# Kernel tuning notes

Hardware: AMD Instinct MI355X
Metric: run time of the kernel (lower is better)

The kernel has to match this reference:

```python
import jax, jax.numpy as jnp
import numpy as np

N_ENTITIES = 300000
N_ITEMS = 150000
N_USERS = 150000
N_EDGES = 2000000
N_INTER = 2000000
N_REL = 32
D = 64


def _scatter_mean(src, index, dim_size):
    # torch_scatter.scatter_mean: sum per segment divided by count; empty segments -> 0
    sums = jax.ops.segment_sum(src, index, num_segments=dim_size)
    cnt = jax.ops.segment_sum(jnp.ones((src.shape[0],), src.dtype), index, num_segments=dim_size)
    return sums / jnp.maximum(cnt, 1.0)[:, None]


def setup_inputs() -> dict:
    key = jax.random.key(0)
    ks = jax.random.split(key, 9)
    return {
        "entity_emb": jax.random.normal(ks[0], (N_ENTITIES, D), dtype=jnp.float32),
        "user_emb": jax.random.normal(ks[1], (N_USERS, D), dtype=jnp.float32),
        "edge_index": jax.random.randint(ks[2], (2, N_EDGES), 0, N_ENTITIES),
        "edge_type": jax.random.randint(ks[3], (N_EDGES,), 0, N_REL),
        "mat_row": jax.random.randint(ks[4], (N_INTER,), 0, N_USERS),
        "mat_col": jax.random.randint(ks[5], (N_INTER,), 0, N_ITEMS),
        "weight": jax.random.normal(ks[6], (N_REL, D), dtype=jnp.float32),
        "gate1_w": jax.random.normal(ks[7], (D, D), dtype=jnp.float32) * 0.1,
        "gate2_w": jax.random.normal(ks[8], (D, D), dtype=jnp.float32) * 0.1,
    }


def reference(entity_emb, user_emb, edge_index, edge_type, mat_row, mat_col, weight, gate1_w, gate2_w):
    head, tail = edge_index[0], edge_index[1]
    # KG aggregation: gather tail embeddings, modulate by relation emb, scatter-mean to head
    neigh_relation_emb = entity_emb[tail] * weight[edge_type]          # [E, D]
    entity_kg_agg = _scatter_mean(neigh_relation_emb, head, N_ENTITIES)
    item_kg_agg = entity_kg_agg[:N_ITEMS]                              # [I, D]
    att_kg_agg = entity_kg_agg[N_ITEMS:]                               # [Ent-I, D]
    # interaction aggregation: gather user emb by row, scatter-mean to item (col)
    item_int_agg = _scatter_mean(user_emb[mat_row], mat_col, N_ITEMS)  # [I, D]
    # gated fusion (F.linear: x @ W.T)
    gi = jax.nn.sigmoid(item_kg_agg @ gate1_w.T + item_int_agg @ gate2_w.T)
    item_emb_fusion = gi * item_kg_agg + (1.0 - gi) * item_int_agg
    # sparse mm with all-ones values == segment sum of fused item embs over users
    user_agg = jax.ops.segment_sum(item_emb_fusion[mat_col], mat_row, num_segments=N_USERS)
    final_entity_agg = jnp.concatenate([item_emb_fusion, att_kg_agg], axis=0)
    return (final_entity_agg, user_agg, item_kg_agg, item_int_agg)
```

## Files before the change

kernel.cpp:

```cpp
#include <hip/hip_runtime.h>

#define N_ENTITIES 300000
#define N_ITEMS    150000
#define N_USERS    150000
#define N_EDGES    2000000
#define N_INTER    2000000
#define D          64
#define N_TOT      (N_ENTITIES + N_ITEMS + N_USERS)

__global__ void hist_ent_kernel(const int* __restrict__ head,
                                int* __restrict__ cnt,
                                int* __restrict__ r_ent) {
    int e = blockIdx.x * 256 + threadIdx.x;
    if (e >= N_EDGES) return;
    r_ent[e] = atomicAdd(&cnt[head[e]], 1);
}

__global__ void hist_item_kernel(const int* __restrict__ mat_col,
                                 int* __restrict__ cnt,
                                 int* __restrict__ r_item) {
    int e = blockIdx.x * 256 + threadIdx.x;
    if (e >= N_INTER) return;
    r_item[e] = atomicAdd(&cnt[N_ENTITIES + mat_col[e]], 1);
}

__global__ void hist_user_kernel(const int* __restrict__ mat_row,
                                 int* __restrict__ cnt,
                                 int* __restrict__ r_user) {
    int e = blockIdx.x * 256 + threadIdx.x;
    if (e >= N_INTER) return;
    r_user[e] = atomicAdd(&cnt[N_ENTITIES + N_ITEMS + mat_row[e]], 1);
}

__global__ void transpose_gates_kernel(const float* __restrict__ g1,
                                       const float* __restrict__ g2,
                                       float* __restrict__ g1t,
                                       float* __restrict__ g2t) {
    int i = blockIdx.x * 256 + threadIdx.x;
    if (i >= 64 * 64) return;
    int o = i >> 6, k = i & 63;
    g1t[k * 64 + o] = g1[i];
    g2t[k * 64 + o] = g2[i];
}

__global__ __launch_bounds__(256) void scan_partial(const int* __restrict__ in,
                                                    int* __restrict__ incl,
                                                    int* __restrict__ bsums,
                                                    int n) {
    __shared__ int lds[256];
    int t = threadIdx.x;
    int base = blockIdx.x * 1024 + t * 4;
    int v0 = (base + 0 < n) ? in[base + 0] : 0;
    int v1 = (base + 1 < n) ? in[base + 1] : 0;
    int v2 = (base + 2 < n) ? in[base + 2] : 0;
    int v3 = (base + 3 < n) ? in[base + 3] : 0;
    int s = v0 + v1 + v2 + v3;
    lds[t] = s;
    __syncthreads();
    for (int off = 1; off < 256; off <<= 1) {
        int x = (t >= off) ? lds[t - off] : 0;
        __syncthreads();
        lds[t] += x;
        __syncthreads();
    }
    int excl = lds[t] - s;
    if (base + 0 < n) incl[base + 0] = excl + v0;
    if (base + 1 < n) incl[base + 1] = excl + v0 + v1;
    if (base + 2 < n) incl[base + 2] = excl + v0 + v1 + v2;
    if (base + 3 < n) incl[base + 3] = excl + s;
    if (t == 255) bsums[blockIdx.x] = lds[255];
}

__global__ __launch_bounds__(1024) void scan_bsums(int* __restrict__ bsums, int nb) {
    __shared__ int lds[1024];
    int t = threadIdx.x;
    lds[t] = (t < nb) ? bsums[t] : 0;
    __syncthreads();
    for (int off = 1; off < 1024; off <<= 1) {
        int x = (t >= off) ? lds[t - off] : 0;
        __syncthreads();
        lds[t] += x;
        __syncthreads();
    }
    if (t < nb) bsums[t] = lds[t];
}

__global__ void scan_finalize(const int* __restrict__ incl,
                              const int* __restrict__ bsums,
                              int* __restrict__ off_ent,
                              int* __restrict__ off_item,
                              int* __restrict__ off_user) {
    int i = blockIdx.x * 256 + threadIdx.x;
    if (i >= N_TOT) return;
    int b = i >> 10;
    int g = incl[i] + ((b > 0) ? bsums[b - 1] : 0);
    if (i < N_ENTITIES) {
        off_ent[i + 1] = g;
        if (i == 0) { off_ent[0] = 0; }
    } else if (i < N_ENTITIES + N_ITEMS) {
        off_item[i - N_ENTITIES + 1] = g - N_EDGES;
        if (i == N_ENTITIES) { off_item[0] = 0; }
    } else {
        off_user[i - N_ENTITIES - N_ITEMS + 1] = g - 2 * N_EDGES;
        if (i == N_ENTITIES + N_ITEMS) { off_user[0] = 0; }
    }
}

__global__ void scatter_ent_kernel(const int* __restrict__ head,
                                   const int* __restrict__ tail,
                                   const int* __restrict__ type,
                                   const int* __restrict__ r_ent,
                                   const int* __restrict__ off_ent,
                                   int* __restrict__ tt_sorted) {
    int e = blockIdx.x * 256 + threadIdx.x;
    if (e >= N_EDGES) return;
    int pos = off_ent[head[e]] + r_ent[e];
    __builtin_nontemporal_store(tail[e] | (type[e] << 19), &tt_sorted[pos]);
}

__global__ void scatter_item_kernel(const int* __restrict__ mat_col,
                                    const int* __restrict__ mat_row,
                                    const int* __restrict__ r_item,
                                    const int* __restrict__ off_item,
                                    int* __restrict__ row_sorted) {
    int e = blockIdx.x * 256 + threadIdx.x;
    if (e >= N_INTER) return;
    int pos = off_item[mat_col[e]] + r_item[e];
    __builtin_nontemporal_store(mat_row[e], &row_sorted[pos]);
}

__global__ void scatter_user_kernel(const int* __restrict__ mat_row,
                                    const int* __restrict__ mat_col,
                                    const int* __restrict__ r_user,
                                    const int* __restrict__ off_user,
                                    int* __restrict__ col_sorted) {
    int e = blockIdx.x * 256 + threadIdx.x;
    if (e >= N_INTER) return;
    int pos = off_user[mat_row[e]] + r_user[e];
    __builtin_nontemporal_store(mat_col[e], &col_sorted[pos]);
}

__global__ __launch_bounds__(256, 8) void agg_ent_kernel(
        const float* __restrict__ entity_emb, const float* __restrict__ weight,
        const int* __restrict__ off, const int* __restrict__ tt_sorted,
        float* __restrict__ out_item_kg, float* __restrict__ out_final) {
    int wave = threadIdx.x >> 6, lane = threadIdx.x & 63;
    int g = lane >> 4, q = lane & 15;
    int ent = blockIdx.x * 4 + wave;
    if (ent >= N_ENTITIES) return;
    int s = off[ent], e = off[ent + 1];
    int cnt = e - s;
    const float4* __restrict__ emb4 = (const float4*)entity_emb;
    const float4* __restrict__ wt4  = (const float4*)weight;
    float ax = 0.f, ay = 0.f, az = 0.f, aw = 0.f;
    for (int idx = s + g; idx < e; idx += 8) {
        int v0 = tt_sorted[idx];
        int i2 = idx + 4;
        bool p2 = (i2 < e);
        int v1 = p2 ? tt_sorted[i2] : 0;
        {
            int t = v0 & 0x7FFFF, w = v0 >> 19;
            float4 a = emb4[t * 16 + q];
            float4 b = wt4[w * 16 + q];
            ax += a.x * b.x; ay += a.y * b.y; az += a.z * b.z; aw += a.w * b.w;
        }
        if (p2) {
            int t = v1 & 0x7FFFF, w = v1 >> 19;
            float4 a = emb4[t * 16 + q];
            float4 b = wt4[w * 16 + q];
            ax += a.x * b.x; ay += a.y * b.y; az += a.z * b.z; aw += a.w * b.w;
        }
    }
    ax += __shfl_xor(ax, 16); ax += __shfl_xor(ax, 32);
    ay += __shfl_xor(ay, 16); ay += __shfl_xor(ay, 32);
    az += __shfl_xor(az, 16); az += __shfl_xor(az, 32);
    aw += __shfl_xor(aw, 16); aw += __shfl_xor(aw, 32);
    if (g == 0) {
        float inv = 1.0f / (float)(cnt > 1 ? cnt : 1);
        float4 r; r.x = ax * inv; r.y = ay * inv; r.z = az * inv; r.w = aw * inv;
        if (ent < N_ITEMS) ((float4*)out_item_kg)[ent * 16 + q] = r;
        else               ((float4*)out_final)[ent * 16 + q]   = r;
    }
}

__global__ __launch_bounds__(512, 6) void agg_item_fuse_kernel(
        const float* __restrict__ user_emb,
        const int* __restrict__ off, const int* __restrict__ row_sorted,
        const float* __restrict__ item_kg,
        const float* __restrict__ g1t, const float* __restrict__ g2t,
        float* __restrict__ out_item_int, float* __restrict__ out_final) {
    __shared__ float s_g1t[4096];
    __shared__ float s_g2t[4096];
    __shared__ float s_ii[8 * 64];

    {
        const float4* a = (const float4*)g1t;
        const float4* b = (const float4*)g2t;
        float4* sa = (float4*)s_g1t;
        float4* sb = (float4*)s_g2t;
        #pragma unroll
        for (int i = threadIdx.x; i < 1024; i += 512) { sa[i] = a[i]; sb[i] = b[i]; }
    }

    int wave = threadIdx.x >> 6, lane = threadIdx.x & 63;
    int g = lane >> 4, q = lane & 15;
    int item = blockIdx.x * 8 + wave;
    int s = off[item], e = off[item + 1];
    int cnt = e - s;
    const float4* __restrict__ ue4 = (const float4*)user_emb;
    float ax = 0.f, ay = 0.f, az = 0.f, aw = 0.f;
    for (int idx = s + g; idx < e; idx += 8) {
        int r0 = row_sorted[idx];
        int i2 = idx + 4;
        bool p2 = (i2 < e);
        int r1 = p2 ? row_sorted[i2] : 0;
        {
            float4 v = ue4[r0 * 16 + q];
            ax += v.x; ay += v.y; az += v.z; aw += v.w;
        }
        if (p2) {
            float4 v = ue4[r1 * 16 + q];
            ax += v.x; ay += v.y; az += v.z; aw += v.w;
        }
    }
    ax += __shfl_xor(ax, 16); ax += __shfl_xor(ax, 32);
    ay += __shfl_xor(ay, 16); ay += __shfl_xor(ay, 32);
    az += __shfl_xor(az, 16); az += __shfl_xor(az, 32);
    aw += __shfl_xor(aw, 16); aw += __shfl_xor(aw, 32);
    float inv = 1.0f / (float)(cnt > 1 ? cnt : 1);
    ax *= inv; ay *= inv; az *= inv; aw *= inv;
    if (g == 0) {
        float4 t; t.x = ax; t.y = ay; t.z = az; t.w = aw;
        *(float4*)&s_ii[wave * 64 + 4 * q] = t;
    }
    __syncthreads();

    const float* __restrict__ kgrow = item_kg + (long long)item * 64;
    float gx = 0.f, gy = 0.f, gz = 0.f, gw = 0.f;
    #pragma unroll 4
    for (int i = 0; i < 16; ++i) {
        int k = 16 * g + i;
        float kk = kgrow[k];
        float ik = s_ii[wave * 64 + k];
        float4 w1 = *(const float4*)&s_g1t[k * 64 + 4 * q];
        float4 w2 = *(const float4*)&s_g2t[k * 64 + 4 * q];
        gx += kk * w1.x + ik * w2.x;
        gy += kk * w1.y + ik * w2.y;
        gz += kk * w1.z + ik * w2.z;
        gw += kk * w1.w + ik * w2.w;
    }
    gx += __shfl_xor(gx, 16); gx += __shfl_xor(gx, 32);
    gy += __shfl_xor(gy, 16); gy += __shfl_xor(gy, 32);
    gz += __shfl_xor(gz, 16); gz += __shfl_xor(gz, 32);
    gw += __shfl_xor(gw, 16); gw += __shfl_xor(gw, 32);

    if (g == 0) {
        float4 kg4 = *(const float4*)&kgrow[4 * q];
        float4 ii4; ii4.x = ax; ii4.y = ay; ii4.z = az; ii4.w = aw;
        float4 o;
        float s0 = 1.0f / (1.0f + __expf(-gx)); o.x = s0 * kg4.x + (1.0f - s0) * ii4.x;
        float s1 = 1.0f / (1.0f + __expf(-gy)); o.y = s1 * kg4.y + (1.0f - s1) * ii4.y;
        float s2 = 1.0f / (1.0f + __expf(-gz)); o.z = s2 * kg4.z + (1.0f - s2) * ii4.z;
        float s3 = 1.0f / (1.0f + __expf(-gw)); o.w = s3 * kg4.w + (1.0f - s3) * ii4.w;
        ((float4*)out_item_int)[item * 16 + q] = ii4;
        ((float4*)out_final)[item * 16 + q]    = o;
    }
}

__global__ __launch_bounds__(256, 8) void agg_user_kernel(
        const float* __restrict__ fusion,
        const int* __restrict__ off, const int* __restrict__ col_sorted,
        float* __restrict__ out_user) {
    int wave = threadIdx.x >> 6, lane = threadIdx.x & 63;
    int g = lane >> 4, q = lane & 15;
    int user = blockIdx.x * 4 + wave;
    if (user >= N_USERS) return;
    int s = off[user], e = off[user + 1];
    const float4* __restrict__ f4 = (const float4*)fusion;
    float ax = 0.f, ay = 0.f, az = 0.f, aw = 0.f;
    for (int idx = s + g; idx < e; idx += 8) {
        int c0 = col_sorted[idx];
        int i2 = idx + 4;
        bool p2 = (i2 < e);
        int c1 = p2 ? col_sorted[i2] : 0;
        {
            float4 v = f4[c0 * 16 + q];
            ax += v.x; ay += v.y; az += v.z; aw += v.w;
        }
        if (p2) {
            float4 v = f4[c1 * 16 + q];
            ax += v.x; ay += v.y; az += v.z; aw += v.w;
        }
    }
    ax += __shfl_xor(ax, 16); ax += __shfl_xor(ax, 32);
    ay += __shfl_xor(ay, 16); ay += __shfl_xor(ay, 32);
    az += __shfl_xor(az, 16); az += __shfl_xor(az, 32);
    aw += __shfl_xor(aw, 16); aw += __shfl_xor(aw, 32);
    if (g == 0) {
        float4 r; r.x = ax; r.y = ay; r.z = az; r.w = aw;
        ((float4*)out_user)[user * 16 + q] = r;
    }
}


extern "C" void kernel_launch(void* const* d_in, const int* in_sizes, int n_in,
                              void* d_out, int out_size, void* d_ws, size_t ws_size,
                              hipStream_t stream) {
    const float* entity_emb = (const float*)d_in[0];
    const float* user_emb   = (const float*)d_in[1];
    const int*   edge_index = (const int*)d_in[2];
    const int*   edge_type  = (const int*)d_in[3];
    const int*   mat_row    = (const int*)d_in[4];
    const int*   mat_col    = (const int*)d_in[5];
    const float* weight     = (const float*)d_in[6];
    const float* g1         = (const float*)d_in[7];
    const float* g2         = (const float*)d_in[8];

    const int* edge_head = edge_index;
    const int* edge_tail = edge_index + N_EDGES;

    float* out = (float*)d_out;
    float* out_final    = out;
    float* out_user     = out + (long long)N_ENTITIES * D;
    float* out_item_kg  = out_user + (long long)N_USERS * D;
    float* out_item_int = out_item_kg + (long long)N_ITEMS * D;

    int* w = (int*)d_ws;
    float* g1t_glob = (float*)w;  w += 64 * 64;
    float* g2t_glob = (float*)w;  w += 64 * 64;
    int* cnt       = w;  w += N_TOT;
    int* off_ent   = w;  w += N_ENTITIES + 1;
    int* off_item  = w;  w += N_ITEMS + 1;
    int* off_user  = w;  w += N_USERS + 1;
    int* incl_tmp  = w;  w += N_TOT;
    int* bsums     = w;  w += 1024;
    int* r_ent     = w;  w += N_EDGES;
    int* r_item    = w;  w += N_INTER;
    int* r_user    = w;  w += N_INTER;
    int* tt_sorted = w;  w += N_EDGES;
    int* row_sorted= w;  w += N_INTER;
    int* col_sorted= w;  w += N_INTER;

    hipMemsetAsync(cnt, 0, (size_t)N_TOT * sizeof(int), stream);

    const int EB = (N_EDGES + 255) / 256;

    transpose_gates_kernel<<<16, 256, 0, stream>>>(g1, g2, g1t_glob, g2t_glob);

    hist_ent_kernel <<<EB, 256, 0, stream>>>(edge_head, cnt, r_ent);
    hist_item_kernel<<<EB, 256, 0, stream>>>(mat_col,  cnt, r_item);
    hist_user_kernel<<<EB, 256, 0, stream>>>(mat_row,  cnt, r_user);

    {
        int nb = (N_TOT + 1023) / 1024;
        scan_partial<<<nb, 256, 0, stream>>>(cnt, incl_tmp, bsums, N_TOT);
        scan_bsums<<<1, 1024, 0, stream>>>(bsums, nb);
        scan_finalize<<<(N_TOT + 255) / 256, 256, 0, stream>>>(
            incl_tmp, bsums, off_ent, off_item, off_user);
    }

    scatter_ent_kernel <<<EB, 256, 0, stream>>>(edge_head, edge_tail, edge_type,
                                                r_ent, off_ent, tt_sorted);
    scatter_item_kernel<<<EB, 256, 0, stream>>>(mat_col, mat_row,
                                                r_item, off_item, row_sorted);
    scatter_user_kernel<<<EB, 256, 0, stream>>>(mat_row, mat_col,
                                                r_user, off_user, col_sorted);

    agg_ent_kernel<<<N_ENTITIES / 4, 256, 0, stream>>>(
        entity_emb, weight, off_ent, tt_sorted, out_item_kg, out_final);
    agg_item_fuse_kernel<<<N_ITEMS / 8, 512, 0, stream>>>(
        user_emb, off_item, row_sorted, out_item_kg, g1t_glob, g2t_glob,
        out_item_int, out_final);
    agg_user_kernel<<<N_USERS / 4, 256, 0, stream>>>(
        out_final, off_user, col_sorted, out_user);
}
```

Measured before the change: 1.046 ms.

## Unroll masked gathers four-deep and make item-fusion blocks persistent

The three aggregation kernels now gather four neighbours per lane-group per iteration instead of two. Tail iterations clamp the index and multiply the extra terms by a 0/1 mask rather than branching, so more independent loads are in flight. The item-fusion kernel becomes persistent: 1250 blocks each process 120 items, so the two 64x64 gate matrices are loaded into shared memory once per block rather than once per 8 items. The item_kg row is read once as a float4 and broadcast with shuffles for the gate matvec. Launch-bound occupancy hints are lowered for the entity and user kernels. The risks are register pressure from the wider unroll and loss of parallelism from the smaller item grid.

Result: slower. 1.516 ms (+44.9%).

```diff
diff --git a/kernel.cpp b/kernel.cpp
--- a/kernel.cpp
+++ b/kernel.cpp
@@ -140,36 +140,35 @@
     __builtin_nontemporal_store(mat_col[e], &col_sorted[pos]);
 }
 
-__global__ __launch_bounds__(256, 8) void agg_ent_kernel(
+__global__ __launch_bounds__(256, 4) void agg_ent_kernel(
         const float* __restrict__ entity_emb, const float* __restrict__ weight,
         const int* __restrict__ off, const int* __restrict__ tt_sorted,
         float* __restrict__ out_item_kg, float* __restrict__ out_final) {
     int wave = threadIdx.x >> 6, lane = threadIdx.x & 63;
     int g = lane >> 4, q = lane & 15;
     int ent = blockIdx.x * 4 + wave;
-    if (ent >= N_ENTITIES) return;
     int s = off[ent], e = off[ent + 1];
     int cnt = e - s;
     const float4* __restrict__ emb4 = (const float4*)entity_emb;
     const float4* __restrict__ wt4  = (const float4*)weight;
     float ax = 0.f, ay = 0.f, az = 0.f, aw = 0.f;
-    for (int idx = s + g; idx < e; idx += 8) {
+    for (int idx = s + g; idx < e; idx += 16) {
+        int j1 = idx + 4,  j2 = idx + 8,  j3 = idx + 12;
+        float m1 = (j1 < e) ? 1.f : 0.f;  j1 = (j1 < e) ? j1 : e - 1;
+        float m2 = (j2 < e) ? 1.f : 0.f;  j2 = (j2 < e) ? j2 : e - 1;
+        float m3 = (j3 < e) ? 1.f : 0.f;  j3 = (j3 < e) ? j3 : e - 1;
         int v0 = tt_sorted[idx];
-        int i2 = idx + 4;
-        bool p2 = (i2 < e);
-        int v1 = p2 ? tt_sorted[i2] : 0;
-        {
-            int t = v0 & 0x7FFFF, w = v0 >> 19;
-            float4 a = emb4[t * 16 + q];
-            float4 b = wt4[w * 16 + q];
-            ax += a.x * b.x; ay += a.y * b.y; az += a.z * b.z; aw += a.w * b.w;
-        }
-        if (p2) {
-            int t = v1 & 0x7FFFF, w = v1 >> 19;
-            float4 a = emb4[t * 16 + q];
-            float4 b = wt4[w * 16 + q];
-            ax += a.x * b.x; ay += a.y * b.y; az += a.z * b.z; aw += a.w * b.w;
-        }
+        int v1 = tt_sorted[j1];
+        int v2 = tt_sorted[j2];
+        int v3 = tt_sorted[j3];
+        float4 a0 = emb4[(v0 & 0x7FFFF) * 16 + q], b0 = wt4[(v0 >> 19) * 16 + q];
+        float4 a1 = emb4[(v1 & 0x7FFFF) * 16 + q], b1 = wt4[(v1 >> 19) * 16 + q];
+        float4 a2 = emb4[(v2 & 0x7FFFF) * 16 + q], b2 = wt4[(v2 >> 19) * 16 + q];
+        float4 a3 = emb4[(v3 & 0x7FFFF) * 16 + q], b3 = wt4[(v3 >> 19) * 16 + q];
+        ax += a0.x * b0.x + m1 * (a1.x * b1.x) + m2 * (a2.x * b2.x) + m3 * (a3.x * b3.x);
+        ay += a0.y * b0.y + m1 * (a1.y * b1.y) + m2 * (a2.y * b2.y) + m3 * (a3.y * b3.y);
+        az += a0.z * b0.z + m1 * (a1.z * b1.z) + m2 * (a2.z * b2.z) + m3 * (a3.z * b3.z);
+        aw += a0.w * b0.w + m1 * (a1.w * b1.w) + m2 * (a2.w * b2.w) + m3 * (a3.w * b3.w);
     }
     ax += __shfl_xor(ax, 16); ax += __shfl_xor(ax, 32);
     ay += __shfl_xor(ay, 16); ay += __shfl_xor(ay, 32);
@@ -183,6 +182,8 @@
     }
 }
 
+#define ITEM_BLOCKS   1250
+#define ITEMS_PER_BLK 120
 __global__ __launch_bounds__(512, 6) void agg_item_fuse_kernel(
         const float* __restrict__ user_emb,
         const int* __restrict__ off, const int* __restrict__ row_sorted,
@@ -191,7 +192,7 @@
         float* __restrict__ out_item_int, float* __restrict__ out_final) {
     __shared__ float s_g1t[4096];
     __shared__ float s_g2t[4096];
-    __shared__ float s_ii[8 * 64];
+    __shared__ float s_ii[8][64];
 
     {
         const float4* a = (const float4*)g1t;
@@ -201,96 +202,108 @@
         #pragma unroll
         for (int i = threadIdx.x; i < 1024; i += 512) { sa[i] = a[i]; sb[i] = b[i]; }
     }
+    __syncthreads();
 
     int wave = threadIdx.x >> 6, lane = threadIdx.x & 63;
     int g = lane >> 4, q = lane & 15;
-    int item = blockIdx.x * 8 + wave;
-    int s = off[item], e = off[item + 1];
-    int cnt = e - s;
     const float4* __restrict__ ue4 = (const float4*)user_emb;
-    float ax = 0.f, ay = 0.f, az = 0.f, aw = 0.f;
-    for (int idx = s + g; idx < e; idx += 8) {
-        int r0 = row_sorted[idx];
-        int i2 = idx + 4;
-        bool p2 = (i2 < e);
-        int r1 = p2 ? row_sorted[i2] : 0;
-        {
-            float4 v = ue4[r0 * 16 + q];
-            ax += v.x; ay += v.y; az += v.z; aw += v.w;
+
+    for (int it = 0; it < ITEMS_PER_BLK / 8; ++it) {
+        int item = blockIdx.x * ITEMS_PER_BLK + it * 8 + wave;
+        int s = off[item], e = off[item + 1];
+        int cnt = e - s;
+        float ax = 0.f, ay = 0.f, az = 0.f, aw = 0.f;
+        for (int idx = s + g; idx < e; idx += 16) {
+            int j1 = idx + 4,  j2 = idx + 8,  j3 = idx + 12;
+            float m1 = (j1 < e) ? 1.f : 0.f;  j1 = (j1 < e) ? j1 : e - 1;
+            float m2 = (j2 < e) ? 1.f : 0.f;  j2 = (j2 < e) ? j2 : e - 1;
+            float m3 = (j3 < e) ? 1.f : 0.f;  j3 = (j3 < e) ? j3 : e - 1;
+            int r0 = row_sorted[idx];
+            int r1 = row_sorted[j1];
+            int r2 = row_sorted[j2];
+            int r3 = row_sorted[j3];
+            float4 v0 = ue4[r0 * 16 + q];
+            float4 v1 = ue4[r1 * 16 + q];
+            float4 v2 = ue4[r2 * 16 + q];
+            float4 v3 = ue4[r3 * 16 + q];
+            ax += v0.x + m1 * v1.x + m2 * v2.x + m3 * v3.x;
+            ay += v0.y + m1 * v1.y + m2 * v2.y + m3 * v3.y;
+            az += v0.z + m1 * v1.z + m2 * v2.z + m3 * v3.z;
+            aw += v0.w + m1 * v1.w + m2 * v2.w + m3 * v3.w;
         }
-        if (p2) {
-            float4 v = ue4[r1 * 16 + q];
-            ax += v.x; ay += v.y; az += v.z; aw += v.w;
+        ax += __shfl_xor(ax, 16); ax += __shfl_xor(ax, 32);
+        ay += __shfl_xor(ay, 16); ay += __shfl_xor(ay, 32);
+        az += __shfl_xor(az, 16); az += __shfl_xor(az, 32);
+        aw += __shfl_xor(aw, 16); aw += __shfl_xor(aw, 32);
+        float inv = 1.0f / (float)(cnt > 1 ? cnt : 1);
+        ax *= inv; ay *= inv; az *= inv; aw *= inv;
+        if (g == 0) {
+            float4 t; t.x = ax; t.y = ay; t.z = az; t.w = aw;
+            *(float4*)&s_ii[wave][4 * q] = t;
         }
-    }
-    ax += __shfl_xor(ax, 16); ax += __shfl_xor(ax, 32);
-    ay += __shfl_xor(ay, 16); ay += __shfl_xor(ay, 32);
-    az += __shfl_xor(az, 16); az += __shfl_xor(az, 32);
-    aw += __shfl_xor(aw, 16); aw += __shfl_xor(aw, 32);
-    float inv = 1.0f / (float)(cnt > 1 ? cnt : 1);
-    ax *= inv; ay *= inv; az *= inv; aw *= inv;
-    if (g == 0) {
-        float4 t; t.x = ax; t.y = ay; t.z = az; t.w = aw;
-        *(float4*)&s_ii[wave * 64 + 4 * q] = t;
-    }
-    __syncthreads();
-
-    const float* __restrict__ kgrow = item_kg + (long long)item * 64;
-    float gx = 0.f, gy = 0.f, gz = 0.f, gw = 0.f;
-    #pragma unroll 4
-    for (int i = 0; i < 16; ++i) {
-        int k = 16 * g + i;
-        float kk = kgrow[k];
-        float ik = s_ii[wave * 64 + k];
-        float4 w1 = *(const float4*)&s_g1t[k * 64 + 4 * q];
-        float4 w2 = *(const float4*)&s_g2t[k * 64 + 4 * q];
-        gx += kk * w1.x + ik * w2.x;
-        gy += kk * w1.y + ik * w2.y;
-        gz += kk * w1.z + ik * w2.z;
-        gw += kk * w1.w + ik * w2.w;
-    }
-    gx += __shfl_xor(gx, 16); gx += __shfl_xor(gx, 32);
-    gy += __shfl_xor(gy, 16); gy += __shfl_xor(gy, 32);
-    gz += __shfl_xor(gz, 16); gz += __shfl_xor(gz, 32);
-    gw += __shfl_xor(gw, 16); gw += __shfl_xor(gw, 32);
-
-    if (g == 0) {
-        float4 kg4 = *(const float4*)&kgrow[4 * q];
-        float4 ii4; ii4.x = ax; ii4.y = ay; ii4.z = az; ii4.w = aw;
-        float4 o;
-        float s0 = 1.0f / (1.0f + __expf(-gx)); o.x = s0 * kg4.x + (1.0f - s0) * ii4.x;
-        float s1 = 1.0f / (1.0f + __expf(-gy)); o.y = s1 * kg4.y + (1.0f - s1) * ii4.y;
-        float s2 = 1.0f / (1.0f + __expf(-gz)); o.z = s2 * kg4.z + (1.0f - s2) * ii4.z;
-        float s3 = 1.0f / (1.0f + __expf(-gw)); o.w = s3 * kg4.w + (1.0f - s3) * ii4.w;
-        ((float4*)out_item_int)[item * 16 + q] = ii4;
-        ((float4*)out_final)[item * 16 + q]    = o;
-    }
-}
-
-__global__ __launch_bounds__(256, 8) void agg_user_kernel(
+
+        float4 kg4 = ((const float4*)item_kg)[item * 16 + q];
+
+        float gx = 0.f, gy = 0.f, gz = 0.f, gw = 0.f;
+        #pragma unroll
+        for (int i = 0; i < 16; ++i) {
+            int k = 16 * g + i;
+            float kgsel = ((i & 3) == 0) ? kg4.x : ((i & 3) == 1) ? kg4.y
+                        : ((i & 3) == 2) ? kg4.z : kg4.w;
+            float kk = __shfl(kgsel, 4 * g + (i >> 2));
+            float ik = s_ii[wave][k];
+            float4 w1 = *(const float4*)&s_g1t[k * 64 + 4 * q];
+            float4 w2 = *(const float4*)&s_g2t[k * 64 + 4 * q];
+            gx += kk * w1.x + ik * w2.x;
+            gy += kk * w1.y + ik * w2.y;
+            gz += kk * w1.z + ik * w2.z;
+            gw += kk * w1.w + ik * w2.w;
+        }
+        gx += __shfl_xor(gx, 16); gx += __shfl_xor(gx, 32);
+        gy += __shfl_xor(gy, 16); gy += __shfl_xor(gy, 32);
+        gz += __shfl_xor(gz, 16); gz += __shfl_xor(gz, 32);
+        gw += __shfl_xor(gw, 16); gw += __shfl_xor(gw, 32);
+
+        if (g == 0) {
+            float4 ii4; ii4.x = ax; ii4.y = ay; ii4.z = az; ii4.w = aw;
+            float4 o;
+            float s0 = 1.0f / (1.0f + __expf(-gx)); o.x = s0 * kg4.x + (1.0f - s0) * ii4.x;
+            float s1 = 1.0f / (1.0f + __expf(-gy)); o.y = s1 * kg4.y + (1.0f - s1) * ii4.y;
+            float s2 = 1.0f / (1.0f + __expf(-gz)); o.z = s2 * kg4.z + (1.0f - s2) * ii4.z;
+            float s3 = 1.0f / (1.0f + __expf(-gw)); o.w = s3 * kg4.w + (1.0f - s3) * ii4.w;
+            ((float4*)out_item_int)[item * 16 + q] = ii4;
+            ((float4*)out_final)[item * 16 + q]    = o;
+        }
+    }
+}
+
+__global__ __launch_bounds__(256, 4) void agg_user_kernel(
         const float* __restrict__ fusion,
         const int* __restrict__ off, const int* __restrict__ col_sorted,
         float* __restrict__ out_user) {
     int wave = threadIdx.x >> 6, lane = threadIdx.x & 63;
     int g = lane >> 4, q = lane & 15;
     int user = blockIdx.x * 4 + wave;
-    if (user >= N_USERS) return;
     int s = off[user], e = off[user + 1];
     const float4* __restrict__ f4 = (const float4*)fusion;
     float ax = 0.f, ay = 0.f, az = 0.f, aw = 0.f;
-    for (int idx = s + g; idx < e; idx += 8) {
+    for (int idx = s + g; idx < e; idx += 16) {
+        int j1 = idx + 4,  j2 = idx + 8,  j3 = idx + 12;
+        float m1 = (j1 < e) ? 1.f : 0.f;  j1 = (j1 < e) ? j1 : e - 1;
+        float m2 = (j2 < e) ? 1.f : 0.f;  j2 = (j2 < e) ? j2 : e - 1;
+        float m3 = (j3 < e) ? 1.f : 0.f;  j3 = (j3 < e) ? j3 : e - 1;
         int c0 = col_sorted[idx];
-        int i2 = idx + 4;
-        bool p2 = (i2 < e);
-        int c1 = p2 ? col_sorted[i2] : 0;
-        {
-            float4 v = f4[c0 * 16 + q];
-            ax += v.x; ay += v.y; az += v.z; aw += v.w;
-        }
-        if (p2) {
-            float4 v = f4[c1 * 16 + q];
-            ax += v.x; ay += v.y; az += v.z; aw += v.w;
-        }
+        int c1 = col_sorted[j1];
+        int c2 = col_sorted[j2];
+        int c3 = col_sorted[j3];
+        float4 v0 = f4[c0 * 16 + q];
+        float4 v1 = f4[c1 * 16 + q];
+        float4 v2 = f4[c2 * 16 + q];
+        float4 v3 = f4[c3 * 16 + q];
+        ax += v0.x + m1 * v1.x + m2 * v2.x + m3 * v3.x;
+        ay += v0.y + m1 * v1.y + m2 * v2.y + m3 * v3.y;
+        az += v0.z + m1 * v1.z + m2 * v2.z + m3 * v3.z;
+        aw += v0.w + m1 * v1.w + m2 * v2.w + m3 * v3.w;
     }
     ax += __shfl_xor(ax, 16); ax += __shfl_xor(ax, 32);
     ay += __shfl_xor(ay, 16); ay += __shfl_xor(ay, 32);
@@ -368,7 +381,7 @@
 
     agg_ent_kernel<<<N_ENTITIES / 4, 256, 0, stream>>>(
         entity_emb, weight, off_ent, tt_sorted, out_item_kg, out_final);
-    agg_item_fuse_kernel<<<N_ITEMS / 8, 512, 0, stream>>>(
+    agg_item_fuse_kernel<<<ITEM_BLOCKS, 512, 0, stream>>>(
         user_emb, off_item, row_sorted, out_item_kg, g1t_glob, g2t_glob,
         out_item_int, out_final);
     agg_user_kernel<<<N_USERS / 4, 256, 0, stream>>>(
```
